# Performance work log

Hardware: AMD Instinct MI355X
Metric: run time of the kernel (lower is better)

Reference implementation:

```python
import jax, jax.numpy as jnp
import numpy as np

WIN_SIZE = 256           # GlobalConfig.win_size (assumed)
NFFT = 2 * WIN_SIZE      # 512 -> NFREQ = 257 rfft bins
HOP = WIN_SIZE
NFREQ = WIN_SIZE + 1
K = 3                    # all kernel sizes in the model
EPS = 1e-5


def _stft(x):
    # x: (B, S) -> (B, T, F, 2) real view of complex STFT (hann window, no center)
    B, S = x.shape
    T = (S - NFFT) // HOP + 1
    n = jnp.arange(NFFT)
    win = 0.5 - 0.5 * jnp.cos(2.0 * jnp.pi * n / NFFT)
    idx = jnp.arange(T)[:, None] * HOP + n[None, :]
    frames = x[:, idx] * win                       # (B, T, NFFT)
    spec = jnp.fft.rfft(frames, axis=-1)           # (B, T, F) complex
    return jnp.stack([spec.real, spec.imag], axis=-1).astype(x.dtype)


def _td_layer(x, W, b, same):
    # time-distributed conv over the frequency axis. x: (B,T,F,Cin), W: (k,Cin,Cout)
    k = W.shape[0]
    if same:
        x = jnp.pad(x, ((0, 0), (0, 0), (k // 2, k - 1 - k // 2), (0, 0)))
    Fout = x.shape[2] - k + 1
    xs = jnp.stack([x[:, :, i:i + Fout] for i in range(k)], axis=0)  # (k,B,T,Fout,Cin)
    return jnp.einsum('kbtfc,kco->btfo', xs, W) + b


def _td_block(x, W1, b1, W2, b2):
    h = jax.nn.relu(_td_layer(x, W1, b1, True))
    return _td_layer(h, W2, b2, True)


def _layer(x, g, beta, dw, W1, b1, W2, b2):
    # LayerNorm over (F, C), causal depthwise conv over T, TD pointwise block, ReLU
    B, T, F, C = x.shape
    mu = x.mean(axis=(-2, -1), keepdims=True)
    var = x.var(axis=(-2, -1), keepdims=True)
    xn = (x - mu) * jax.lax.rsqrt(var + EPS) * g + beta
    h = xn.reshape(B, T, F * C)
    hp = jnp.pad(h, ((0, 0), (K - 1, 0), (0, 0)))   # causal left-pad on time
    y = sum(hp[:, i:i + T, :] * dw[:, i] for i in range(K))  # (B,T,F*C) depthwise
    y = y.reshape(B, T, F, C)
    return jax.nn.relu(_td_block(y, W1, b1, W2, b2))


def setup_inputs() -> dict:
    key = jax.random.key(0)
    ks = iter(jax.random.split(key, 40))
    def rn(shape, s=0.05):
        return (jax.random.normal(next(ks), shape) * s).astype(jnp.float32)
    F = NFREQ
    d = {}
    d['x'] = jax.random.normal(next(ks), (8, 262144), dtype=jnp.float32)
    d['l0_W1'] = rn((3, 2, 4)); d['l0_b1'] = jnp.zeros((4,), jnp.float32)
    d['l0_W2'] = rn((3, 4, 8)); d['l0_b2'] = jnp.zeros((8,), jnp.float32)
    for name, cin in (('l1', 8), ('l2', 16), ('l3', 24)):
        d[name + '_g'] = jnp.ones((F, cin), jnp.float32)
        d[name + '_bn'] = jnp.zeros((F, cin), jnp.float32)
        d[name + '_dw'] = rn((F * cin, 3), 0.3)
        d[name + '_W1'] = rn((3, cin, 8)); d[name + '_b1'] = jnp.zeros((8,), jnp.float32)
        d[name + '_W2'] = rn((3, 8, 8)); d[name + '_b2'] = jnp.zeros((8,), jnp.float32)
    d['fc1_W'] = rn((3, 32, 1)); d['fc1_b'] = jnp.zeros((1,), jnp.float32)
    d['fc2_W'] = rn((F - 2, 1)); d['fc2_b'] = jnp.zeros((1,), jnp.float32)
    return d


def reference(x, l0_W1, l0_b1, l0_W2, l0_b2,
              l1_g, l1_bn, l1_dw, l1_W1, l1_b1, l1_W2, l1_b2,
              l2_g, l2_bn, l2_dw, l2_W1, l2_b1, l2_W2, l2_b2,
              l3_g, l3_bn, l3_dw, l3_W1, l3_b1, l3_W2, l3_b2,
              fc1_W, fc1_b, fc2_W, fc2_b):
    s = _stft(x)                                            # (B,T,F,2)
    h = jax.nn.relu(_td_block(s, l0_W1, l0_b1, l0_W2, l0_b2))  # (B,T,F,8)
    h = jnp.concatenate([h, _layer(h, l1_g, l1_bn, l1_dw, l1_W1, l1_b1, l1_W2, l1_b2)], axis=3)
    h = jnp.concatenate([h, _layer(h, l2_g, l2_bn, l2_dw, l2_W1, l2_b1, l2_W2, l2_b2)], axis=3)
    h = jnp.concatenate([h, _layer(h, l3_g, l3_bn, l3_dw, l3_W1, l3_b1, l3_W2, l3_b2)], axis=3)
    h = jax.nn.relu(_td_layer(h, fc1_W, fc1_b, False))[..., 0]  # (B,T,F-2)
    out = jax.nn.sigmoid(h @ fc2_W + fc2_b)                 # (B,T,1)
    return out[..., 0]                                      # (B,T)
```

## Files before the change

kernel.cpp:

```cpp
#include <hip/hip_runtime.h>
#include <hip/hip_fp16.h>

namespace {

constexpr int BATCH = 8;
constexpr int SLEN  = 262144;
constexpr int TT    = 1023;
constexpr int NF    = 257;
constexpr int NCH   = 24;
constexpr int NBT   = BATCH * TT;
constexpr int FRS   = NCH * NF;
constexpr float EPS = 1e-5f;

__device__ inline int div257(int e) { return (e * 65282) >> 24; }

__global__ __launch_bounds__(256, 8) void stft_l0_kernel(
    const float* __restrict__ x,
    const float* __restrict__ W1g, const float* __restrict__ b1g,
    const float* __restrict__ W2g, const float* __restrict__ b2g,
    __half* __restrict__ H, float* __restrict__ stats0)
{
  __shared__ float  xw[512];
  __shared__ __align__(16) float2 ab[256];
  __shared__ float  sre[NF + 2];
  __shared__ float  sim[NF + 2];
  __shared__ float  h1[4][NF + 2];
  __shared__ float  wW1[24], wb1[4], wW2[96], wb2[8];
  __shared__ float  red[8];

  const int tid = threadIdx.x;
  const int bt  = blockIdx.x;
  const int b   = bt / TT;
  const int t   = bt - b * TT;
  const float* xp = x + (size_t)b * SLEN + (size_t)t * 256;

  if (tid < 24) wW1[tid] = W1g[tid];
  if (tid < 4)  wb1[tid] = b1g[tid];
  if (tid < 96) wW2[tid] = W2g[tid];
  if (tid < 8)  wb2[tid] = b2g[tid];

  const float STEP = 6.283185307179586f / 512.0f;
  for (int n = tid; n < 512; n += 256) {
    float sv, cv;
    sincosf(STEP * (float)n, &sv, &cv);
    xw[n] = xp[n] * (0.5f - 0.5f * cv);
  }
  __syncthreads();

  if (tid == 0) ab[0] = make_float2(0.f, 0.f);
  if (tid >= 1) {
    float u = xw[tid], v = xw[512 - tid];
    ab[tid] = make_float2(u + v, u - v);
  }
  __syncthreads();

  const float x0 = xw[0], x256 = xw[256];

  if (tid < 128) {
    const int k = tid;
    float s1, c1;
    sincosf(STEP * (float)k, &s1, &c1);
    const float c2 = fmaf(c1, c1, -s1 * s1), s2 = 2.f * c1 * s1;
    const float c3 = fmaf(c2, c1, -s2 * s1), s3 = fmaf(c2, s1, s2 * c1);
    const float c4 = fmaf(c2, c2, -s2 * s2), s4 = 2.f * c2 * s2;
    float cA = 1.f, sA = 0.f;
    float cB = c1,  sB = s1;
    float cC = c2,  sC = s2;
    float cD = c3,  sD = s3;
    float re_e = 0.f, re_o = 0.f, im_e = 0.f, im_o = 0.f;
    const float4* ab4 = (const float4*)ab;
    for (int m = 0; m < 64; ++m) {
      const float4 q0 = ab4[2 * m];
      const float4 q1 = ab4[2 * m + 1];
      re_e = fmaf(q0.x, cA, re_e); im_e = fmaf(q0.y, sA, im_e);
      re_o = fmaf(q0.z, cB, re_o); im_o = fmaf(q0.w, sB, im_o);
      re_e = fmaf(q1.x, cC, re_e); im_e = fmaf(q1.y, sC, im_e);
      re_o = fmaf(q1.z, cD, re_o); im_o = fmaf(q1.w, sD, im_o);
      float t0;
      t0 = fmaf(cA, c4, -sA * s4); sA = fmaf(cA, s4, sA * c4); cA = t0;
      t0 = fmaf(cB, c4, -sB * s4); sB = fmaf(cB, s4, sB * c4); cB = t0;
      t0 = fmaf(cC, c4, -sC * s4); sC = fmaf(cC, s4, sC * c4); cC = t0;
      t0 = fmaf(cD, c4, -sD * s4); sD = fmaf(cD, s4, sD * c4); cD = t0;
    }
    const float rb = x0 + ((k & 1) ? -x256 : x256);
    sre[1 + k] = rb + re_e + re_o;
    sim[1 + k] = -(im_e + im_o);
    sre[1 + 256 - k] = rb + re_e - re_o;
    sim[1 + 256 - k] = im_e - im_o;
  } else {
    const int m = tid - 128;
    const float sgn = (m & 1) ? -1.f : 1.f;
    float tr = ab[2 * m].x * sgn;
    float ti = -ab[2 * m + 1].y * sgn;
    #pragma unroll
    for (int off = 32; off > 0; off >>= 1) {
      tr += __shfl_down(tr, off, 64);
      ti += __shfl_down(ti, off, 64);
    }
    if ((tid & 63) == 0) {
      const int w = (tid >> 6) - 2;
      red[w * 2] = tr; red[w * 2 + 1] = ti;
    }
  }
  __syncthreads();
  if (tid == 0) {
    sre[1 + 128] = x0 + x256 + red[0] + red[2];
    sim[1 + 128] = red[1] + red[3];
    sre[0] = 0.f; sim[0] = 0.f; sre[258] = 0.f; sim[258] = 0.f;
  }
  __syncthreads();

  for (int f = tid; f < NF; f += 256) {
    float acc[4] = {wb1[0], wb1[1], wb1[2], wb1[3]};
    #pragma unroll
    for (int i = 0; i < 3; ++i) {
      float vr = sre[f + i], vi = sim[f + i];
      #pragma unroll
      for (int c = 0; c < 4; ++c)
        acc[c] = fmaf(vr, wW1[(i*2+0)*4 + c], fmaf(vi, wW1[(i*2+1)*4 + c], acc[c]));
    }
    #pragma unroll
    for (int c = 0; c < 4; ++c) h1[c][f + 1] = fmaxf(acc[c], 0.f);
  }
  if (tid < 4) { h1[tid][0] = 0.f; h1[tid][NF + 1] = 0.f; }
  __syncthreads();

  const size_t obase = (size_t)bt * FRS;
  float ps1 = 0.f, ps2 = 0.f;
  for (int f = tid; f < NF; f += 256) {
    float acc[8];
    #pragma unroll
    for (int c = 0; c < 8; ++c) acc[c] = wb2[c];
    #pragma unroll
    for (int i = 0; i < 3; ++i)
      #pragma unroll
      for (int c4 = 0; c4 < 4; ++c4) {
        float hv = h1[c4][f + i];
        #pragma unroll
        for (int c = 0; c < 8; ++c)
          acc[c] = fmaf(hv, wW2[(i*4+c4)*8 + c], acc[c]);
      }
    #pragma unroll
    for (int c = 0; c < 8; ++c) {
      const __half hv = __float2half(fmaxf(acc[c], 0.f));
      H[obase + (size_t)c * NF + f] = hv;
      const float v = __half2float(hv);
      ps1 += v;
      ps2 = fmaf(v, v, ps2);
    }
  }
  #pragma unroll
  for (int off = 32; off > 0; off >>= 1) {
    ps1 += __shfl_down(ps1, off, 64);
    ps2 += __shfl_down(ps2, off, 64);
  }
  if ((tid & 63) == 0) { red[(tid >> 6) * 2] = ps1; red[(tid >> 6) * 2 + 1] = ps2; }
  __syncthreads();
  if (tid == 0) {
    stats0[bt * 2]     = red[0] + red[2] + red[4] + red[6];
    stats0[bt * 2 + 1] = red[1] + red[3] + red[5] + red[7];
  }
}

template<int CIN>
__global__ __launch_bounds__(256) void fold_tbl(
    const float* __restrict__ g, const float* __restrict__ bn,
    const float* __restrict__ dw, __half* __restrict__ dst)
{
  constexpr int NEL = CIN * NF;
  const int idx = blockIdx.x * 256 + threadIdx.x;
  if (idx >= NEL) return;
  const int c = div257(idx), f = idx - c * 257;
  const int s = f * CIN + c;
  const float gv = g[s], bv = bn[s];
  const float d0 = dw[s * 3], d1 = dw[s * 3 + 1], d2 = dw[s * 3 + 2];
  dst[idx]           = __float2half(gv * d0);
  dst[NEL + idx]     = __float2half(gv * d1);
  dst[2 * NEL + idx] = __float2half(gv * d2);
  dst[3 * NEL + idx] = __float2half(bv * (d0 + d1 + d2));
  dst[4 * NEL + idx] = __float2half(bv * (d1 + d2));
  dst[5 * NEL + idx] = __float2half(bv * d2);
}

template<int CIN, bool HEAD>
__global__ __launch_bounds__(256, 8) void layer_bt(
    const __half* __restrict__ H, __half* __restrict__ Hout,
    const float* __restrict__ st0, const float* __restrict__ st1,
    const float* __restrict__ st2, float* __restrict__ stats_out,
    const __half* __restrict__ tbl,
    const float* __restrict__ W1g, const float* __restrict__ b1g,
    const float* __restrict__ W2g, const float* __restrict__ b2g,
    const float* __restrict__ fc1W, const float* __restrict__ fc1b,
    const float* __restrict__ fc2W, const float* __restrict__ fc2b,
    float* __restrict__ out)
{
  constexpr int NEL   = CIN * NF;
  constexpr int NP2   = NEL / 2;
  constexpr int NPER2 = (NP2 + 255) / 256;
  constexpr int TAIL2 = NP2 - 256 * (NPER2 - 1);

  __shared__ __half y[CIN * 259];
  __shared__ __half h1[8 * 259];
  __shared__ float wW1[3 * CIN * 8], wb1[8], wW2[192], wb2[8];
  __shared__ float red[8];
  __shared__ float wfc1[HEAD ? 96 : 1];

  const int tid = threadIdx.x;
  const int bt  = blockIdx.x;
  const int b   = bt / TT;
  const int t   = bt - b * TT;

  const __half hz = __float2half(0.f);
  for (int i = tid; i < 3 * CIN * 8; i += 256) wW1[i] = W1g[i];
  if (tid < 192) wW2[tid] = W2g[tid];
  if (tid < 8) { wb1[tid] = b1g[tid]; wb2[tid] = b2g[tid]; }
  if (tid < CIN) { y[tid * 259] = hz; y[tid * 259 + 258] = hz; }
  if (tid < 8)   { h1[tid * 259] = hz; h1[tid * 259 + 258] = hz; }
  if constexpr (HEAD) { if (tid < 96) wfc1[tid] = fc1W[tid]; }

  float mu0 = 0.f, rs0 = 0.f, mu1 = 0.f, rs1 = 0.f, mu2, rs2;
  {
    const float inv = 1.0f / (float)NEL;
    float s1 = st0[bt * 2], s2v = st0[bt * 2 + 1];
    if constexpr (CIN >= 16) { s1 += st1[bt * 2]; s2v += st1[bt * 2 + 1]; }
    if constexpr (CIN >= 24) { s1 += st2[bt * 2]; s2v += st2[bt * 2 + 1]; }
    mu2 = s1 * inv; rs2 = rsqrtf(s2v * inv - mu2 * mu2 + EPS);
    if (t >= 1) {
      const int fb = bt - 1;
      float a = st0[fb * 2], c = st0[fb * 2 + 1];
      if constexpr (CIN >= 16) { a += st1[fb * 2]; c += st1[fb * 2 + 1]; }
      if constexpr (CIN >= 24) { a += st2[fb * 2]; c += st2[fb * 2 + 1]; }
      mu1 = a * inv; rs1 = rsqrtf(c * inv - mu1 * mu1 + EPS);
    }
    if (t >= 2) {
      const int fb = bt - 2;
      float a = st0[fb * 2], c = st0[fb * 2 + 1];
      if constexpr (CIN >= 16) { a += st1[fb * 2]; c += st1[fb * 2 + 1]; }
      if constexpr (CIN >= 24) { a += st2[fb * 2]; c += st2[fb * 2 + 1]; }
      mu0 = a * inv; rs0 = rsqrtf(c * inv - mu0 * mu0 + EPS);
    }
  }

  const int base = b * TT;
  const __half2* f2p = (const __half2*)(H + (size_t)bt * FRS);
  const __half2* f1p = (const __half2*)(H + (size_t)max(bt - 1, base) * FRS);
  const __half2* f0p = (const __half2*)(H + (size_t)max(bt - 2, base) * FRS);
  const __half2* P0p = (const __half2*)tbl;
  const __half2* P1p = (const __half2*)(tbl + NEL);
  const __half2* P2p = (const __half2*)(tbl + 2 * NEL);
  const int qsel = (t >= 2) ? 0 : (t == 1 ? 1 : 2);
  const __half2* Qp  = (const __half2*)(tbl + (3 + qsel) * NEL);

  #pragma unroll
  for (int j = 0; j < NPER2; ++j) {
    const bool act = (j < NPER2 - 1) || (tid < TAIL2);
    if (act) {
      const int p  = tid + 256 * j;
      const int e0 = 2 * p;
      const int c0 = div257(e0);
      const int fi = e0 - c0 * 257;
      const float2 xa = __half22float2(f0p[p]);
      const float2 xb = __half22float2(f1p[p]);
      const float2 xc = __half22float2(f2p[p]);
      const float2 pa = __half22float2(P0p[p]);
      const float2 pb = __half22float2(P1p[p]);
      const float2 pc = __half22float2(P2p[p]);
      const float2 qq = __half22float2(Qp[p]);
      const float y0 = fmaf((xa.x - mu0) * rs0, pa.x,
                       fmaf((xb.x - mu1) * rs1, pb.x,
                       fmaf((xc.x - mu2) * rs2, pc.x, qq.x)));
      const float y1 = fmaf((xa.y - mu0) * rs0, pa.y,
                       fmaf((xb.y - mu1) * rs1, pb.y,
                       fmaf((xc.y - mu2) * rs2, pc.y, qq.y)));
      const int a0 = c0 * 259 + 1 + fi;
      y[a0] = __float2half(y0);
      y[a0 + ((fi == 256) ? 3 : 1)] = __float2half(y1);
    }
  }
  __syncthreads();

  {
    const int f = tid;
    float acc[8];
    #pragma unroll
    for (int c = 0; c < 8; ++c) acc[c] = wb1[c];
    #pragma unroll
    for (int i = 0; i < 3; ++i)
      for (int cin = 0; cin < CIN; ++cin) {
        const float yv = __half2float(y[cin * 259 + f + i]);
        #pragma unroll
        for (int c = 0; c < 8; ++c)
          acc[c] = fmaf(yv, wW1[(i * CIN + cin) * 8 + c], acc[c]);
      }
    #pragma unroll
    for (int c = 0; c < 8; ++c)
      h1[c * 259 + 1 + f] = __float2half(fmaxf(acc[c], 0.f));
  }
  if (tid < 8) {
    float a = wb1[tid];
    #pragma unroll
    for (int i = 0; i < 3; ++i)
      for (int cin = 0; cin < CIN; ++cin)
        a = fmaf(__half2float(y[cin * 259 + 256 + i]), wW1[(i * CIN + cin) * 8 + tid], a);
    h1[tid * 259 + 257] = __float2half(fmaxf(a, 0.f));
  }
  __syncthreads();

  __half* out2 = y;
  float ps1 = 0.f, ps2 = 0.f;
  {
    const int f = tid;
    float o2[8];
    #pragma unroll
    for (int c = 0; c < 8; ++c) o2[c] = wb2[c];
    #pragma unroll
    for (int i = 0; i < 3; ++i)
      #pragma unroll
      for (int c8 = 0; c8 < 8; ++c8) {
        const float hv = __half2float(h1[c8 * 259 + f + i]);
        #pragma unroll
        for (int c = 0; c < 8; ++c)
          o2[c] = fmaf(hv, wW2[(i * 8 + c8) * 8 + c], o2[c]);
      }
    if constexpr (!HEAD) {
      const size_t ob = (size_t)bt * FRS + (size_t)CIN * NF;
      #pragma unroll
      for (int c = 0; c < 8; ++c) {
        const __half hv = __float2half(fmaxf(o2[c], 0.f));
        Hout[ob + (size_t)c * NF + f] = hv;
        const float v = __half2float(hv);
        ps1 += v;
        ps2 = fmaf(v, v, ps2);
      }
    } else {
      #pragma unroll
      for (int c = 0; c < 8; ++c)
        out2[c * 257 + f] = __float2half(fmaxf(o2[c], 0.f));
    }
  }
  if (tid >= 8 && tid < 16) {
    const int c8 = tid - 8;
    float a = wb2[c8];
    #pragma unroll
    for (int i = 0; i < 3; ++i)
      #pragma unroll
      for (int cp = 0; cp < 8; ++cp)
        a = fmaf(__half2float(h1[cp * 259 + 256 + i]), wW2[(i * 8 + cp) * 8 + c8], a);
    if constexpr (!HEAD) {
      const size_t ob = (size_t)bt * FRS + (size_t)CIN * NF;
      const __half hv = __float2half(fmaxf(a, 0.f));
      Hout[ob + (size_t)c8 * NF + 256] = hv;
      const float v = __half2float(hv);
      ps1 += v;
      ps2 = fmaf(v, v, ps2);
    } else {
      out2[c8 * 257 + 256] = __float2half(fmaxf(a, 0.f));
    }
  }

  if constexpr (!HEAD) {
    #pragma unroll
    for (int off = 32; off > 0; off >>= 1) {
      ps1 += __shfl_down(ps1, off, 64);
      ps2 += __shfl_down(ps2, off, 64);
    }
    if ((tid & 63) == 0) { red[(tid >> 6) * 2] = ps1; red[(tid >> 6) * 2 + 1] = ps2; }
    __syncthreads();
    if (tid == 0) {
      stats_out[bt * 2]     = red[0] + red[2] + red[4] + red[6];
      stats_out[bt * 2 + 1] = red[1] + red[3] + red[5] + red[7];
    }
  } else {
    __syncthreads();
    float part = 0.f;
    if (tid < NF - 2) {
      const __half* xg = (const __half*)f2p;
      float acc = fc1b[0];
      #pragma unroll
      for (int i = 0; i < 3; ++i) {
        for (int c = 0; c < 24; ++c)
          acc = fmaf(__half2float(xg[c * 257 + tid + i]), wfc1[i * 32 + c], acc);
        #pragma unroll
        for (int c8 = 0; c8 < 8; ++c8)
          acc = fmaf(__half2float(out2[c8 * 257 + tid + i]), wfc1[i * 32 + 24 + c8], acc);
      }
      part = fmaxf(acc, 0.f) * fc2W[tid];
    }
    #pragma unroll
    for (int off = 32; off > 0; off >>= 1) part += __shfl_down(part, off, 64);
    if ((tid & 63) == 0) red[tid >> 6] = part;
    __syncthreads();
    if (tid == 0) {
      const float tot = red[0] + red[1] + red[2] + red[3] + fc2b[0];
      out[bt] = 1.0f / (1.0f + expf(-tot));
    }
  }
}

}

extern "C" void kernel_launch(void* const* d_in, const int* in_sizes, int n_in,
                              void* d_out, int out_size, void* d_ws, size_t ws_size,
                              hipStream_t stream) {
  (void)in_sizes; (void)n_in; (void)out_size; (void)ws_size;
  const float* x = (const float*)d_in[0];
  float* out = (float*)d_out;
  char*  wsb = (char*)d_ws;

  __half* H   = (__half*)wsb;
  char* p = wsb + (size_t)NBT * FRS * sizeof(__half);
  float* st0  = (float*)p; p += 2 * NBT * sizeof(float);
  float* st1  = (float*)p; p += 2 * NBT * sizeof(float);
  float* st2  = (float*)p; p += 2 * NBT * sizeof(float);
  __half* tbl1 = (__half*)p; p += 6 * (8  * NF) * sizeof(__half);
  __half* tbl2 = (__half*)p; p += 6 * (16 * NF) * sizeof(__half);
  __half* tbl3 = (__half*)p;

  dim3 blk(256);

  fold_tbl<8><<<dim3((8 * NF + 255) / 256), blk, 0, stream>>>(
      (const float*)d_in[5], (const float*)d_in[6], (const float*)d_in[7], tbl1);
  fold_tbl<16><<<dim3((16 * NF + 255) / 256), blk, 0, stream>>>(
      (const float*)d_in[12], (const float*)d_in[13], (const float*)d_in[14], tbl2);
  fold_tbl<24><<<dim3((24 * NF + 255) / 256), blk, 0, stream>>>(
      (const float*)d_in[19], (const float*)d_in[20], (const float*)d_in[21], tbl3);

  stft_l0_kernel<<<dim3(NBT), blk, 0, stream>>>(
      x, (const float*)d_in[1], (const float*)d_in[2],
      (const float*)d_in[3], (const float*)d_in[4], H, st0);

  layer_bt<8, false><<<dim3(NBT), blk, 0, stream>>>(
      H, H, st0, nullptr, nullptr, st1, tbl1,
      (const float*)d_in[8], (const float*)d_in[9],
      (const float*)d_in[10], (const float*)d_in[11],
      nullptr, nullptr, nullptr, nullptr, nullptr);

  layer_bt<16, false><<<dim3(NBT), blk, 0, stream>>>(
      H, H, st0, st1, nullptr, st2, tbl2,
      (const float*)d_in[15], (const float*)d_in[16],
      (const float*)d_in[17], (const float*)d_in[18],
      nullptr, nullptr, nullptr, nullptr, nullptr);

  layer_bt<24, true><<<dim3(NBT), blk, 0, stream>>>(
      H, nullptr, st0, st1, st2, nullptr, tbl3,
      (const float*)d_in[22], (const float*)d_in[23],
      (const float*)d_in[24], (const float*)d_in[25],
      (const float*)d_in[26], (const float*)d_in[27],
      (const float*)d_in[28], (const float*)d_in[29],
      out);
}
```

Baseline: 442.3 us.

## Use packed fp16 dot2 with transposed LDS layouts and split DFT over all threads

The time-distributed conv layers now keep activations in LDS in a frequency-major, channel-interleaved layout, so pairs of channels can be read as one 32-bit word. They accumulate with the packed fp16 dot2 instruction against pre-packed fp16 weights, which halves the number of multiply-add instructions and LDS reads. The STFT kernel splits the even/odd DFT halves across all 256 threads instead of idling half of them, and the three fold-table launches are merged into one. In exchange, weights are rounded to fp16 and the packed-dot accumulation changes numerics slightly.

```diff
diff --git a/kernel.cpp b/kernel.cpp
--- a/kernel.cpp
+++ b/kernel.cpp
@@ -12,6 +12,24 @@
 constexpr int FRS   = NCH * NF;
 constexpr float EPS = 1e-5f;
 
+typedef _Float16 h2v __attribute__((ext_vector_type(2)));
+
+__device__ inline float fdot2(unsigned a, unsigned b, float c) {
+#if __has_builtin(__builtin_amdgcn_fdot2)
+  return __builtin_amdgcn_fdot2(__builtin_bit_cast(h2v, a),
+                                __builtin_bit_cast(h2v, b), c, false);
+#else
+  h2v av = __builtin_bit_cast(h2v, a), bv = __builtin_bit_cast(h2v, b);
+  return fmaf((float)av[0], (float)bv[0], fmaf((float)av[1], (float)bv[1], c));
+#endif
+}
+__device__ inline unsigned packh2(float a, float b) {
+  h2v v; v[0] = (_Float16)a; v[1] = (_Float16)b;
+  return __builtin_bit_cast(unsigned, v);
+}
+__device__ inline unsigned short f2h(float v) {
+  return __builtin_bit_cast(unsigned short, (_Float16)v);
+}
 __device__ inline int div257(int e) { return (e * 65282) >> 24; }
 
 __global__ __launch_bounds__(256, 8) void stft_l0_kernel(
@@ -21,7 +39,9 @@
     __half* __restrict__ H, float* __restrict__ stats0)
 {
   __shared__ float  xw[512];
-  __shared__ __align__(16) float2 ab[256];
+  __shared__ __align__(16) float2 abE[128];
+  __shared__ __align__(16) float2 abO[128];
+  __shared__ float2 oxc[128];
   __shared__ float  sre[NF + 2];
   __shared__ float  sim[NF + 2];
   __shared__ float  h1[4][NF + 2];
@@ -47,66 +67,79 @@
   }
   __syncthreads();
 
-  if (tid == 0) ab[0] = make_float2(0.f, 0.f);
-  if (tid >= 1) {
-    float u = xw[tid], v = xw[512 - tid];
-    ab[tid] = make_float2(u + v, u - v);
+  if (tid < 128) {
+    const int n = 2 * tid;
+    abE[tid] = (n == 0) ? make_float2(0.f, 0.f)
+                        : make_float2(xw[n] + xw[512 - n], xw[n] - xw[512 - n]);
+  } else {
+    const int n = 2 * (tid - 128) + 1;
+    abO[tid - 128] = make_float2(xw[n] + xw[512 - n], xw[n] - xw[512 - n]);
   }
   __syncthreads();
 
   const float x0 = xw[0], x256 = xw[256];
-
-  if (tid < 128) {
-    const int k = tid;
+  {
+    const int  k = tid & 127;
+    const bool P = (tid >= 128);
     float s1, c1;
     sincosf(STEP * (float)k, &s1, &c1);
-    const float c2 = fmaf(c1, c1, -s1 * s1), s2 = 2.f * c1 * s1;
-    const float c3 = fmaf(c2, c1, -s2 * s1), s3 = fmaf(c2, s1, s2 * c1);
-    const float c4 = fmaf(c2, c2, -s2 * s2), s4 = 2.f * c2 * s2;
-    float cA = 1.f, sA = 0.f;
-    float cB = c1,  sB = s1;
-    float cC = c2,  sC = s2;
-    float cD = c3,  sD = s3;
-    float re_e = 0.f, re_o = 0.f, im_e = 0.f, im_o = 0.f;
-    const float4* ab4 = (const float4*)ab;
-    for (int m = 0; m < 64; ++m) {
-      const float4 q0 = ab4[2 * m];
-      const float4 q1 = ab4[2 * m + 1];
-      re_e = fmaf(q0.x, cA, re_e); im_e = fmaf(q0.y, sA, im_e);
-      re_o = fmaf(q0.z, cB, re_o); im_o = fmaf(q0.w, sB, im_o);
-      re_e = fmaf(q1.x, cC, re_e); im_e = fmaf(q1.y, sC, im_e);
-      re_o = fmaf(q1.z, cD, re_o); im_o = fmaf(q1.w, sD, im_o);
+    const float c2 = fmaf(c1,c1,-s1*s1), s2 = 2.f*c1*s1;
+    const float c3 = fmaf(c2,c1,-s2*s1), s3 = fmaf(c2,s1, s2*c1);
+    const float c4 = fmaf(c2,c2,-s2*s2), s4 = 2.f*c2*s2;
+    const float c5 = fmaf(c4,c1,-s4*s1), s5 = fmaf(c4,s1, s4*c1);
+    const float c6 = fmaf(c4,c2,-s4*s2), s6 = fmaf(c4,s2, s4*c2);
+    const float c7 = fmaf(c4,c3,-s4*s3), s7 = fmaf(c4,s3, s4*c3);
+    const float c8 = fmaf(c4,c4,-s4*s4), s8 = 2.f*c4*s4;
+    float cA = P ? c1 : 1.f, sA = P ? s1 : 0.f;
+    float cB = P ? c3 : c2,  sB = P ? s3 : s2;
+    float cC = P ? c5 : c4,  sC = P ? s5 : s4;
+    float cD = P ? c7 : c6,  sD = P ? s7 : s6;
+    const float4* ab4 = P ? (const float4*)abO : (const float4*)abE;
+    float re = 0.f, im = 0.f;
+    for (int m = 0; m < 32; ++m) {
+      const float4 q0 = ab4[2*m];
+      const float4 q1 = ab4[2*m + 1];
+      re = fmaf(q0.x, cA, re); im = fmaf(q0.y, sA, im);
+      re = fmaf(q0.z, cB, re); im = fmaf(q0.w, sB, im);
+      re = fmaf(q1.x, cC, re); im = fmaf(q1.y, sC, im);
+      re = fmaf(q1.z, cD, re); im = fmaf(q1.w, sD, im);
       float t0;
-      t0 = fmaf(cA, c4, -sA * s4); sA = fmaf(cA, s4, sA * c4); cA = t0;
-      t0 = fmaf(cB, c4, -sB * s4); sB = fmaf(cB, s4, sB * c4); cB = t0;
-      t0 = fmaf(cC, c4, -sC * s4); sC = fmaf(cC, s4, sC * c4); cC = t0;
-      t0 = fmaf(cD, c4, -sD * s4); sD = fmaf(cD, s4, sD * c4); cD = t0;
-    }
-    const float rb = x0 + ((k & 1) ? -x256 : x256);
-    sre[1 + k] = rb + re_e + re_o;
-    sim[1 + k] = -(im_e + im_o);
-    sre[1 + 256 - k] = rb + re_e - re_o;
-    sim[1 + 256 - k] = im_e - im_o;
-  } else {
-    const int m = tid - 128;
-    const float sgn = (m & 1) ? -1.f : 1.f;
-    float tr = ab[2 * m].x * sgn;
-    float ti = -ab[2 * m + 1].y * sgn;
+      t0 = fmaf(cA, c8, -sA*s8); sA = fmaf(cA, s8, sA*c8); cA = t0;
+      t0 = fmaf(cB, c8, -sB*s8); sB = fmaf(cB, s8, sB*c8); cB = t0;
+      t0 = fmaf(cC, c8, -sC*s8); sC = fmaf(cC, s8, sC*c8); cC = t0;
+      t0 = fmaf(cD, c8, -sD*s8); sD = fmaf(cD, s8, sD*c8); cD = t0;
+    }
+    if (P) oxc[k] = make_float2(re, im);
+
+    float tr = 0.f, ti = 0.f;
+    if (tid & 1) {
+      const float v = abO[tid >> 1].y;
+      ti = ((tid >> 1) & 1) ? v : -v;
+    } else {
+      const float v = abE[tid >> 1].x;
+      tr = ((tid >> 1) & 1) ? -v : v;
+    }
     #pragma unroll
     for (int off = 32; off > 0; off >>= 1) {
       tr += __shfl_down(tr, off, 64);
       ti += __shfl_down(ti, off, 64);
     }
-    if ((tid & 63) == 0) {
-      const int w = (tid >> 6) - 2;
-      red[w * 2] = tr; red[w * 2 + 1] = ti;
-    }
-  }
-  __syncthreads();
-  if (tid == 0) {
-    sre[1 + 128] = x0 + x256 + red[0] + red[2];
-    sim[1 + 128] = red[1] + red[3];
-    sre[0] = 0.f; sim[0] = 0.f; sre[258] = 0.f; sim[258] = 0.f;
+    if ((tid & 63) == 0) { red[(tid >> 6)*2] = tr; red[(tid >> 6)*2 + 1] = ti; }
+    __syncthreads();
+
+    if (!P) {
+      const float rb  = x0 + ((k & 1) ? -x256 : x256);
+      const float reo = oxc[k].x, imo = oxc[k].y;
+      sre[1 + k]       = rb + re + reo;
+      sim[1 + k]       = -(im + imo);
+      sre[1 + 256 - k] = rb + re - reo;
+      sim[1 + 256 - k] = im - imo;
+    }
+    if (tid == 0) {
+      sre[1 + 128] = x0 + x256 + red[0] + red[2] + red[4] + red[6];
+      sim[1 + 128] = red[1] + red[3] + red[5] + red[7];
+      sre[0] = 0.f; sim[0] = 0.f; sre[258] = 0.f; sim[258] = 0.f;
+    }
   }
   __syncthreads();
 
@@ -154,6 +187,7 @@
     ps1 += __shfl_down(ps1, off, 64);
     ps2 += __shfl_down(ps2, off, 64);
   }
+  __syncthreads();
   if ((tid & 63) == 0) { red[(tid >> 6) * 2] = ps1; red[(tid >> 6) * 2 + 1] = ps2; }
   __syncthreads();
   if (tid == 0) {
@@ -162,24 +196,31 @@
   }
 }
 
-template<int CIN>
-__global__ __launch_bounds__(256) void fold_tbl(
-    const float* __restrict__ g, const float* __restrict__ bn,
-    const float* __restrict__ dw, __half* __restrict__ dst)
-{
-  constexpr int NEL = CIN * NF;
-  const int idx = blockIdx.x * 256 + threadIdx.x;
-  if (idx >= NEL) return;
+__device__ inline void fold_one(int idx, int CIN,
+    const float* g, const float* bn, const float* dw, __half* dst, int NEL) {
   const int c = div257(idx), f = idx - c * 257;
   const int s = f * CIN + c;
   const float gv = g[s], bv = bn[s];
-  const float d0 = dw[s * 3], d1 = dw[s * 3 + 1], d2 = dw[s * 3 + 2];
-  dst[idx]           = __float2half(gv * d0);
-  dst[NEL + idx]     = __float2half(gv * d1);
-  dst[2 * NEL + idx] = __float2half(gv * d2);
-  dst[3 * NEL + idx] = __float2half(bv * (d0 + d1 + d2));
-  dst[4 * NEL + idx] = __float2half(bv * (d1 + d2));
-  dst[5 * NEL + idx] = __float2half(bv * d2);
+  const float d0 = dw[s*3], d1 = dw[s*3+1], d2 = dw[s*3+2];
+  dst[idx]         = __float2half(gv * d0);
+  dst[NEL + idx]   = __float2half(gv * d1);
+  dst[2*NEL + idx] = __float2half(gv * d2);
+  dst[3*NEL + idx] = __float2half(bv * (d0 + d1 + d2));
+  dst[4*NEL + idx] = __float2half(bv * (d1 + d2));
+  dst[5*NEL + idx] = __float2half(bv * d2);
+}
+
+__global__ __launch_bounds__(256) void fold_all(
+    const float* g1, const float* bn1, const float* dw1, __half* t1,
+    const float* g2, const float* bn2, const float* dw2, __half* t2,
+    const float* g3, const float* bn3, const float* dw3, __half* t3)
+{
+  int idx = blockIdx.x * 256 + threadIdx.x;
+  if (idx < 8*257) { fold_one(idx, 8, g1, bn1, dw1, t1, 8*257); return; }
+  idx -= 8*257;
+  if (idx < 16*257) { fold_one(idx, 16, g2, bn2, dw2, t2, 16*257); return; }
+  idx -= 16*257;
+  if (idx < 24*257) fold_one(idx, 24, g3, bn3, dw3, t3, 24*257);
 }
 
 template<int CIN, bool HEAD>
@@ -198,46 +239,61 @@
   constexpr int NP2   = NEL / 2;
   constexpr int NPER2 = (NP2 + 255) / 256;
   constexpr int TAIL2 = NP2 - 256 * (NPER2 - 1);
-
-  __shared__ __half y[CIN * 259];
-  __shared__ __half h1[8 * 259];
-  __shared__ float wW1[3 * CIN * 8], wb1[8], wW2[192], wb2[8];
+  constexpr int PC1   = CIN + 2;
+  constexpr int PC2   = 10;
+  constexpr int NQ1   = CIN / 2;
+
+  __shared__ unsigned short y_t[259 * PC1];
+  __shared__ unsigned short h1_t[259 * PC2];
+  __shared__ unsigned w1p[3 * NQ1 * 8];
+  __shared__ unsigned w2p[96];
+  __shared__ float wb1[8], wb2[8];
   __shared__ float red[8];
-  __shared__ float wfc1[HEAD ? 96 : 1];
+  __shared__ unsigned wfc1p[HEAD ? 48 : 1];
 
   const int tid = threadIdx.x;
   const int bt  = blockIdx.x;
   const int b   = bt / TT;
   const int t   = bt - b * TT;
 
-  const __half hz = __float2half(0.f);
-  for (int i = tid; i < 3 * CIN * 8; i += 256) wW1[i] = W1g[i];
-  if (tid < 192) wW2[tid] = W2g[tid];
+  for (int idx = tid; idx < 3 * NQ1 * 8; idx += 256) {
+    const int o = idx & 7, q = (idx >> 3) % NQ1, i = idx / (NQ1 * 8);
+    w1p[idx] = packh2(W1g[(i*CIN + 2*q)*8 + o], W1g[(i*CIN + 2*q + 1)*8 + o]);
+  }
+  if (tid < 96) {
+    const int o = tid & 7, q = (tid >> 3) & 3, i = tid >> 5;
+    w2p[tid] = packh2(W2g[(i*8 + 2*q)*8 + o], W2g[(i*8 + 2*q + 1)*8 + o]);
+  }
   if (tid < 8) { wb1[tid] = b1g[tid]; wb2[tid] = b2g[tid]; }
-  if (tid < CIN) { y[tid * 259] = hz; y[tid * 259 + 258] = hz; }
-  if (tid < 8)   { h1[tid * 259] = hz; h1[tid * 259 + 258] = hz; }
-  if constexpr (HEAD) { if (tid < 96) wfc1[tid] = fc1W[tid]; }
+  if (tid < PC1) { y_t[tid] = 0; y_t[258*PC1 + tid] = 0; }
+  if (tid < PC2) { h1_t[tid] = 0; h1_t[258*PC2 + tid] = 0; }
+  if constexpr (HEAD) {
+    if (tid < 48) {
+      const int q = tid & 15, i = tid >> 4;
+      wfc1p[tid] = packh2(fc1W[i*32 + 2*q], fc1W[i*32 + 2*q + 1]);
+    }
+  }
 
   float mu0 = 0.f, rs0 = 0.f, mu1 = 0.f, rs1 = 0.f, mu2, rs2;
   {
     const float inv = 1.0f / (float)NEL;
-    float s1 = st0[bt * 2], s2v = st0[bt * 2 + 1];
-    if constexpr (CIN >= 16) { s1 += st1[bt * 2]; s2v += st1[bt * 2 + 1]; }
-    if constexpr (CIN >= 24) { s1 += st2[bt * 2]; s2v += st2[bt * 2 + 1]; }
-    mu2 = s1 * inv; rs2 = rsqrtf(s2v * inv - mu2 * mu2 + EPS);
+    float s1 = st0[bt*2], s2v = st0[bt*2+1];
+    if constexpr (CIN >= 16) { s1 += st1[bt*2]; s2v += st1[bt*2+1]; }
+    if constexpr (CIN >= 24) { s1 += st2[bt*2]; s2v += st2[bt*2+1]; }
+    mu2 = s1 * inv; rs2 = rsqrtf(s2v * inv - mu2*mu2 + EPS);
     if (t >= 1) {
       const int fb = bt - 1;
-      float a = st0[fb * 2], c = st0[fb * 2 + 1];
-      if constexpr (CIN >= 16) { a += st1[fb * 2]; c += st1[fb * 2 + 1]; }
-      if constexpr (CIN >= 24) { a += st2[fb * 2]; c += st2[fb * 2 + 1]; }
-      mu1 = a * inv; rs1 = rsqrtf(c * inv - mu1 * mu1 + EPS);
+      float a = st0[fb*2], c = st0[fb*2+1];
+      if constexpr (CIN >= 16) { a += st1[fb*2]; c += st1[fb*2+1]; }
+      if constexpr (CIN >= 24) { a += st2[fb*2]; c += st2[fb*2+1]; }
+      mu1 = a * inv; rs1 = rsqrtf(c * inv - mu1*mu1 + EPS);
     }
     if (t >= 2) {
       const int fb = bt - 2;
-      float a = st0[fb * 2], c = st0[fb * 2 + 1];
-      if constexpr (CIN >= 16) { a += st1[fb * 2]; c += st1[fb * 2 + 1]; }
-      if constexpr (CIN >= 24) { a += st2[fb * 2]; c += st2[fb * 2 + 1]; }
-      mu0 = a * inv; rs0 = rsqrtf(c * inv - mu0 * mu0 + EPS);
+      float a = st0[fb*2], c = st0[fb*2+1];
+      if constexpr (CIN >= 16) { a += st1[fb*2]; c += st1[fb*2+1]; }
+      if constexpr (CIN >= 24) { a += st2[fb*2]; c += st2[fb*2+1]; }
+      mu0 = a * inv; rs0 = rsqrtf(c * inv - mu0*mu0 + EPS);
     }
   }
 
@@ -272,9 +328,10 @@
       const float y1 = fmaf((xa.y - mu0) * rs0, pa.y,
                        fmaf((xb.y - mu1) * rs1, pb.y,
                        fmaf((xc.y - mu2) * rs2, pc.y, qq.y)));
-      const int a0 = c0 * 259 + 1 + fi;
-      y[a0] = __float2half(y0);
-      y[a0 + ((fi == 256) ? 3 : 1)] = __float2half(y1);
+      const int a1 = (fi + 1) * PC1 + c0;
+      y_t[a1] = f2h(y0);
+      const int a2 = (fi == 256) ? (PC1 + c0 + 1) : (a1 + PC1);
+      y_t[a2] = f2h(y1);
     }
   }
   __syncthreads();
@@ -284,44 +341,53 @@
     float acc[8];
     #pragma unroll
     for (int c = 0; c < 8; ++c) acc[c] = wb1[c];
-    #pragma unroll
-    for (int i = 0; i < 3; ++i)
-      for (int cin = 0; cin < CIN; ++cin) {
-        const float yv = __half2float(y[cin * 259 + f + i]);
+    const unsigned* yw = (const unsigned*)y_t;
+    #pragma unroll
+    for (int i = 0; i < 3; ++i) {
+      const unsigned* row = yw + (f + i) * (PC1 / 2);
+      for (int q = 0; q < NQ1; ++q) {
+        const unsigned yv = row[q];
         #pragma unroll
         for (int c = 0; c < 8; ++c)
-          acc[c] = fmaf(yv, wW1[(i * CIN + cin) * 8 + c], acc[c]);
+          acc[c] = fdot2(yv, w1p[(i * NQ1 + q) * 8 + c], acc[c]);
       }
-    #pragma unroll
-    for (int c = 0; c < 8; ++c)
-      h1[c * 259 + 1 + f] = __float2half(fmaxf(acc[c], 0.f));
+    }
+    unsigned* hw = (unsigned*)h1_t + (f + 1) * (PC2 / 2);
+    #pragma unroll
+    for (int k = 0; k < 4; ++k)
+      hw[k] = packh2(fmaxf(acc[2*k], 0.f), fmaxf(acc[2*k+1], 0.f));
   }
   if (tid < 8) {
     float a = wb1[tid];
-    #pragma unroll
-    for (int i = 0; i < 3; ++i)
-      for (int cin = 0; cin < CIN; ++cin)
-        a = fmaf(__half2float(y[cin * 259 + 256 + i]), wW1[(i * CIN + cin) * 8 + tid], a);
-    h1[tid * 259 + 257] = __float2half(fmaxf(a, 0.f));
-  }
-  __syncthreads();
-
-  __half* out2 = y;
+    const unsigned* yw = (const unsigned*)y_t;
+    #pragma unroll
+    for (int i = 0; i < 3; ++i) {
+      const unsigned* row = yw + (256 + i) * (PC1 / 2);
+      for (int q = 0; q < NQ1; ++q)
+        a = fdot2(row[q], w1p[(i * NQ1 + q) * 8 + tid], a);
+    }
+    h1_t[257 * PC2 + tid] = f2h(fmaxf(a, 0.f));
+  }
+  __syncthreads();
+
   float ps1 = 0.f, ps2 = 0.f;
   {
     const int f = tid;
     float o2[8];
     #pragma unroll
     for (int c = 0; c < 8; ++c) o2[c] = wb2[c];
-    #pragma unroll
-    for (int i = 0; i < 3; ++i)
-      #pragma unroll
-      for (int c8 = 0; c8 < 8; ++c8) {
-        const float hv = __half2float(h1[c8 * 259 + f + i]);
+    const unsigned* hw = (const unsigned*)h1_t;
+    #pragma unroll
+    for (int i = 0; i < 3; ++i) {
+      const unsigned* row = hw + (f + i) * (PC2 / 2);
+      #pragma unroll
+      for (int q = 0; q < 4; ++q) {
+        const unsigned hv = row[q];
         #pragma unroll
         for (int c = 0; c < 8; ++c)
-          o2[c] = fmaf(hv, wW2[(i * 8 + c8) * 8 + c], o2[c]);
+          o2[c] = fdot2(hv, w2p[(i*4 + q)*8 + c], o2[c]);
       }
+    }
     if constexpr (!HEAD) {
       const size_t ob = (size_t)bt * FRS + (size_t)CIN * NF;
       #pragma unroll
@@ -333,19 +399,23 @@
         ps2 = fmaf(v, v, ps2);
       }
     } else {
-      #pragma unroll
-      for (int c = 0; c < 8; ++c)
-        out2[c * 257 + f] = __float2half(fmaxf(o2[c], 0.f));
+      unsigned* ow = (unsigned*)y_t + f * (PC1 / 2);
+      #pragma unroll
+      for (int k = 0; k < 4; ++k)
+        ow[k] = packh2(fmaxf(o2[2*k], 0.f), fmaxf(o2[2*k+1], 0.f));
     }
   }
   if (tid >= 8 && tid < 16) {
     const int c8 = tid - 8;
     float a = wb2[c8];
-    #pragma unroll
-    for (int i = 0; i < 3; ++i)
-      #pragma unroll
-      for (int cp = 0; cp < 8; ++cp)
-        a = fmaf(__half2float(h1[cp * 259 + 256 + i]), wW2[(i * 8 + cp) * 8 + c8], a);
+    const unsigned* hw = (const unsigned*)h1_t;
+    #pragma unroll
+    for (int i = 0; i < 3; ++i) {
+      const unsigned* row = hw + (256 + i) * (PC2 / 2);
+      #pragma unroll
+      for (int q = 0; q < 4; ++q)
+        a = fdot2(row[q], w2p[(i*4 + q)*8 + c8], a);
+    }
     if constexpr (!HEAD) {
       const size_t ob = (size_t)bt * FRS + (size_t)CIN * NF;
       const __half hv = __float2half(fmaxf(a, 0.f));
@@ -354,7 +424,7 @@
       ps1 += v;
       ps2 = fmaf(v, v, ps2);
     } else {
-      out2[c8 * 257 + 256] = __float2half(fmaxf(a, 0.f));
+      y_t[256 * PC1 + c8] = f2h(fmaxf(a, 0.f));
     }
   }
 
@@ -364,25 +434,30 @@
       ps1 += __shfl_down(ps1, off, 64);
       ps2 += __shfl_down(ps2, off, 64);
     }
-    if ((tid & 63) == 0) { red[(tid >> 6) * 2] = ps1; red[(tid >> 6) * 2 + 1] = ps2; }
+    if ((tid & 63) == 0) { red[(tid >> 6)*2] = ps1; red[(tid >> 6)*2+1] = ps2; }
     __syncthreads();
     if (tid == 0) {
-      stats_out[bt * 2]     = red[0] + red[2] + red[4] + red[6];
-      stats_out[bt * 2 + 1] = red[1] + red[3] + red[5] + red[7];
+      stats_out[bt*2]     = red[0] + red[2] + red[4] + red[6];
+      stats_out[bt*2 + 1] = red[1] + red[3] + red[5] + red[7];
     }
   } else {
     __syncthreads();
     float part = 0.f;
     if (tid < NF - 2) {
-      const __half* xg = (const __half*)f2p;
+      const unsigned short* xgu = (const unsigned short*)f2p;
       float acc = fc1b[0];
       #pragma unroll
       for (int i = 0; i < 3; ++i) {
-        for (int c = 0; c < 24; ++c)
-          acc = fmaf(__half2float(xg[c * 257 + tid + i]), wfc1[i * 32 + c], acc);
+        const int pos = tid + i;
+        for (int q = 0; q < 12; ++q) {
+          const unsigned lo = xgu[(2*q) * 257 + pos];
+          const unsigned hi = xgu[(2*q + 1) * 257 + pos];
+          acc = fdot2(lo | (hi << 16), wfc1p[i*16 + q], acc);
+        }
+        const unsigned* orow = (const unsigned*)y_t + pos * (PC1 / 2);
         #pragma unroll
-        for (int c8 = 0; c8 < 8; ++c8)
-          acc = fmaf(__half2float(out2[c8 * 257 + tid + i]), wfc1[i * 32 + 24 + c8], acc);
+        for (int q = 0; q < 4; ++q)
+          acc = fdot2(orow[q], wfc1p[i*16 + 12 + q], acc);
       }
       part = fmaxf(acc, 0.f) * fc2W[tid];
     }
@@ -418,11 +493,9 @@
 
   dim3 blk(256);
 
-  fold_tbl<8><<<dim3((8 * NF + 255) / 256), blk, 0, stream>>>(
-      (const float*)d_in[5], (const float*)d_in[6], (const float*)d_in[7], tbl1);
-  fold_tbl<16><<<dim3((16 * NF + 255) / 256), blk, 0, stream>>>(
-      (const float*)d_in[12], (const float*)d_in[13], (const float*)d_in[14], tbl2);
-  fold_tbl<24><<<dim3((24 * NF + 255) / 256), blk, 0, stream>>>(
+  fold_all<<<dim3((48 * 257 + 255) / 256), blk, 0, stream>>>(
+      (const float*)d_in[5],  (const float*)d_in[6],  (const float*)d_in[7],  tbl1,
+      (const float*)d_in[12], (const float*)d_in[13], (const float*)d_in[14], tbl2,
       (const float*)d_in[19], (const float*)d_in[20], (const float*)d_in[21], tbl3);
 
   stft_l0_kernel<<<dim3(NBT), blk, 0, stream>>>(
```

Measured after the change: 431.4 us. 2.5% less time.
